# Performance work log

Hardware: AMD Instinct MI355X
Metric: run time of the kernel (lower is better)

Reference implementation:

```python
import jax, jax.numpy as jnp
import numpy as np

B, N1, N2, D = 4, 4096, 4096, 128


def setup_inputs() -> dict:
    key = jax.random.key(0)
    k1, k2 = jax.random.split(key)
    x1 = jax.random.normal(k1, (B, N1, D), dtype=jnp.float32)
    x2 = jax.random.normal(k2, (B, N2, D), dtype=jnp.float32)
    return {"x1": x1, "x2": x2}


def reference(x1, x2):
    # torch.cdist(x2, x1, p=2.0): pairwise euclidean distances [B, N2, N1]
    # Expansion form: ||a||^2 + ||b||^2 - 2 a.b  (single GEMM, no [B,N2,N1,D] intermediate)
    sq2 = jnp.sum(x2 * x2, axis=-1)                      # [B, N2]
    sq1 = jnp.sum(x1 * x1, axis=-1)                      # [B, N1]
    inner = jnp.einsum('bnd,bmd->bnm', x2, x1)           # [B, N2, N1]
    sq = sq2[:, :, None] + sq1[:, None, :] - 2.0 * inner
    corr_mat = jnp.sqrt(jnp.maximum(sq, 0.0))            # clamp numerical negatives
    max_ind21 = jnp.argmin(corr_mat, axis=-1)            # [B, N2] nearest x1 for each x2
    max_ind12 = jnp.argmin(corr_mat, axis=-2)            # [B, N1] nearest x2 for each x1
    return (x1, x2, corr_mat, max_ind12, max_ind21)
```

## Files before the change

kernel.cpp:

```cpp
#include <hip/hip_runtime.h>
#include <stdint.h>
#include <stddef.h>

#define BB 4
#define NN 4096
#define DD 128

typedef _Float16 f16;
typedef _Float16 f16x8 __attribute__((ext_vector_type(8)));
typedef float f32x4 __attribute__((ext_vector_type(4)));

__device__ __forceinline__ void gl16(const f16* g, f16* l) {
  __builtin_amdgcn_global_load_lds(
      (const __attribute__((address_space(1))) unsigned int*)g,
      (__attribute__((address_space(3))) unsigned int*)l,
      16, 0, 0);
}

__device__ __forceinline__ float fast_sqrt(float x) {
  float r;
  asm("v_sqrt_f32 %0, %1" : "=v"(r) : "v"(x));
  return r;
}

__global__ __launch_bounds__(256) void prep_kernel(
    const float* __restrict__ x1, const float* __restrict__ x2,
    f16* __restrict__ x1h, f16* __restrict__ x1l,
    f16* __restrict__ x2h, f16* __restrict__ x2l,
    float* __restrict__ sq1, float* __restrict__ sq2,
    float* __restrict__ out)
{
  int gtid = blockIdx.x * blockDim.x + threadIdx.x;
  int gwave = gtid >> 6;
  int lane = gtid & 63;
  int sub = lane >> 3;
  int j = lane & 7;
  int row = gwave * 8 + sub;
  const float* src; f16* dh; f16* dl; float* sq; float* cpy; int r;
  if (row < BB * NN) {
    r = row; src = x1; dh = x1h; dl = x1l; sq = sq1; cpy = out;
  } else {
    r = row - BB * NN; src = x2; dh = x2h; dl = x2l; sq = sq2;
    cpy = out + (size_t)BB * NN * DD;
  }
  const float* p = src + (size_t)r * DD;
  float acc = 0.0f;
  #pragma unroll
  for (int i = 0; i < DD / 8; ++i) {
    int c = j + i * 8;
    float v = p[c];
    float s = v * v;
    acc = (i == 0) ? s : (acc + s);
    f16 h = (f16)v;
    f16 l = (f16)(v - (float)h);
    dh[(size_t)r * DD + c] = h;
    dl[(size_t)r * DD + c] = l;
    cpy[(size_t)r * DD + c] = v;
  }
  acc = acc + __shfl_xor(acc, 1);
  acc = acc + __shfl_xor(acc, 2);
  acc = acc + __shfl_xor(acc, 4);
  if (j == 0) sq[r] = acc;
}

__global__ __launch_bounds__(512, 4) void cdist_kernel(
    const f16* __restrict__ x1h, const f16* __restrict__ x1l,
    const f16* __restrict__ x2h, const f16* __restrict__ x2l,
    const float* __restrict__ sq1, const float* __restrict__ sq2,
    float* __restrict__ corr,
    float* __restrict__ p21v, int* __restrict__ p21i,
    float* __restrict__ p12v, int* __restrict__ p12i)
{
  __shared__ f16 Ah[128 * 32];
  __shared__ f16 Al[128 * 32];
  __shared__ f16 Bh[128 * 32];
  __shared__ f16 Bl[128 * 32];
  __shared__ float s1s[128];
  __shared__ float s2s[128];

  const int b = blockIdx.z;
  int lin = blockIdx.y * 32 + blockIdx.x;
  lin = (lin & 7) * 128 + (lin >> 3);
  const int sbx = lin & 31;
  const int sby = lin >> 5;
  const int bn1 = sbx * 128;
  const int bn2 = sby * 128;

  const int t = threadIdx.x;
  const int wid = t >> 6;
  const int lane = t & 63;
  const int wm = wid & 1;
  const int wn = wid >> 1;
  const int lr = lane & 15;
  const int lg = lane >> 4;

  const f16* gAh = x1h + (size_t)b * NN * DD;
  const f16* gAl = x1l + (size_t)b * NN * DD;
  const f16* gBh = x2h + (size_t)b * NN * DD;
  const f16* gBl = x2l + (size_t)b * NN * DD;

  if (t < 128) s1s[t] = sq1[(size_t)b * NN + bn1 + t];
  else if (t < 256) s2s[t - 128] = sq2[(size_t)b * NN + bn2 + (t - 128)];

  const int rowc = t >> 2;
  const int kc = (t & 3) ^ (rowc & 3) ^ ((rowc >> 2) & 3);
  const int aoff = bn1 * DD + rowc * DD + kc * 8;
  const int boff = bn2 * DD + rowc * DD + kc * 8;
  const int loff = (wid * 64) * 8;
#define STAGE(k0) do { \
    gl16(gAh + aoff + (k0), &Ah[loff]); \
    gl16(gAl + aoff + (k0), &Al[loff]); \
    gl16(gBh + boff + (k0), &Bh[loff]); \
    gl16(gBl + boff + (k0), &Bl[loff]); } while (0)

  f32x4 acc[4][2];
  #pragma unroll
  for (int m = 0; m < 4; ++m)
    #pragma unroll
    for (int n = 0; n < 2; ++n)
      #pragma unroll
      for (int q = 0; q < 4; ++q) acc[m][n][q] = 0.0f;

  STAGE(0);

  const int lgx8 = (lg ^ (lr & 3) ^ ((lr >> 2) & 3)) * 8;
  const int offA0 = (wm * 64 + lr) * 32 + lgx8;
  const int offB0 = (wn * 32 + lr) * 32 + lgx8;

  for (int it = 0; it < 4; ++it) {
    __syncthreads();
    f16x8 fah[4], fal[4], fbh[2], fbl[2];
    #pragma unroll
    for (int m = 0; m < 4; ++m) {
      fah[m] = *(const f16x8*)&Ah[offA0 + m * 512];
      fal[m] = *(const f16x8*)&Al[offA0 + m * 512];
    }
    #pragma unroll
    for (int n = 0; n < 2; ++n) {
      fbh[n] = *(const f16x8*)&Bh[offB0 + n * 512];
      fbl[n] = *(const f16x8*)&Bl[offB0 + n * 512];
    }
    __syncthreads();
    if (it < 3) STAGE((it + 1) * 32);
    #pragma unroll
    for (int m = 0; m < 4; ++m)
      #pragma unroll
      for (int n = 0; n < 2; ++n) {
        acc[m][n] = __builtin_amdgcn_mfma_f32_16x16x32_f16(fah[m], fbh[n], acc[m][n], 0, 0, 0);
        acc[m][n] = __builtin_amdgcn_mfma_f32_16x16x32_f16(fah[m], fbl[n], acc[m][n], 0, 0, 0);
        acc[m][n] = __builtin_amdgcn_mfma_f32_16x16x32_f16(fal[m], fbh[n], acc[m][n], 0, 0, 0);
      }
  }
#undef STAGE

  float s2r[2];
  #pragma unroll
  for (int n = 0; n < 2; ++n) s2r[n] = s2s[wn * 32 + n * 16 + lr];
  float s1r[4][4];
  #pragma unroll
  for (int m = 0; m < 4; ++m)
    #pragma unroll
    for (int q = 0; q < 4; ++q) s1r[m][q] = s1s[wm * 64 + m * 16 + lg * 4 + q];

  float v21[2]; int i21[2];
  #pragma unroll
  for (int n = 0; n < 2; ++n) { v21[n] = 3.4e38f; i21[n] = 0; }

  float* cbp = corr + (size_t)b * NN * NN;
  #pragma unroll
  for (int m = 0; m < 4; ++m) {
    const int n1b = wm * 64 + m * 16 + lg * 4;
    float v12[4]; int i12[4];
    #pragma unroll
    for (int q = 0; q < 4; ++q) { v12[q] = 3.4e38f; i12[q] = 0; }
    #pragma unroll
    for (int n = 0; n < 2; ++n) {
      const int n2l = wn * 32 + n * 16 + lr;
      f32x4 dv;
      float sqc[4];
      #pragma unroll
      for (int q = 0; q < 4; ++q) {
        const float sv = fmaxf(fmaf(-2.0f, acc[m][n][q], s1r[m][q] + s2r[n]), 0.0f);
        sqc[q] = sv;
        dv[q] = fast_sqrt(sv);
      }
      __builtin_nontemporal_store(dv, (f32x4*)(cbp + (size_t)(bn2 + n2l) * NN + (bn1 + n1b)));
      #pragma unroll
      for (int q = 0; q < 4; ++q) {
        if (sqc[q] < v21[n]) { v21[n] = sqc[q]; i21[n] = bn1 + n1b + q; }
        if (sqc[q] < v12[q]) { v12[q] = sqc[q]; i12[q] = bn2 + n2l; }
      }
    }
    #pragma unroll
    for (int q = 0; q < 4; ++q) {
      float v = v12[q]; int idx = i12[q];
      #pragma unroll
      for (int mask = 1; mask < 16; mask <<= 1) {
        float ov = __shfl_xor(v, mask);
        int oi = __shfl_xor(idx, mask);
        if (ov < v || (ov == v && oi < idx)) { v = ov; idx = oi; }
      }
      if (lr == 0) {
        const int colg = bn1 + n1b + q;
        const size_t o = ((size_t)b * NN + colg) * 128 + (sby * 4 + wn);
        p12v[o] = v; p12i[o] = idx;
      }
    }
  }
  #pragma unroll
  for (int n = 0; n < 2; ++n) {
    float v = v21[n]; int idx = i21[n];
    #pragma unroll
    for (int mask = 16; mask < 64; mask <<= 1) {
      float ov = __shfl_xor(v, mask);
      int oi = __shfl_xor(idx, mask);
      if (ov < v || (ov == v && oi < idx)) { v = ov; idx = oi; }
    }
    if (lg == 0) {
      const int rowg = bn2 + wn * 32 + n * 16 + lr;
      const size_t o = ((size_t)b * NN + rowg) * 64 + (sbx * 2 + wm);
      p21v[o] = v; p21i[o] = idx;
    }
  }
}

__global__ __launch_bounds__(256) void argmin_reduce_kernel(
    const float* __restrict__ p21v, const int* __restrict__ p21i,
    const float* __restrict__ p12v, const int* __restrict__ p12i,
    float* __restrict__ out_i12, float* __restrict__ out_i21)
{
  int gtid = blockIdx.x * blockDim.x + threadIdx.x;
  int gwave = gtid >> 6;
  int lane = gtid & 63;
  float v; int idx; float* dst; int r;
  if (gwave < BB * NN) {
    r = gwave;
    v = p21v[(size_t)r * 64 + lane];
    idx = p21i[(size_t)r * 64 + lane];
    dst = out_i21;
  } else {
    r = gwave - BB * NN;
    v = p12v[(size_t)r * 128 + lane];
    idx = p12i[(size_t)r * 128 + lane];
    float v2 = p12v[(size_t)r * 128 + 64 + lane];
    int i2 = p12i[(size_t)r * 128 + 64 + lane];
    if (v2 < v || (v2 == v && i2 < idx)) { v = v2; idx = i2; }
    dst = out_i12;
  }
  #pragma unroll
  for (int mask = 1; mask < 64; mask <<= 1) {
    float ov = __shfl_xor(v, mask);
    int oi = __shfl_xor(idx, mask);
    if (ov < v || (ov == v && oi < idx)) { v = ov; idx = oi; }
  }
  if (lane == 0) dst[r] = (float)idx;
}

extern "C" void kernel_launch(void* const* d_in, const int* in_sizes, int n_in,
                              void* d_out, int out_size, void* d_ws, size_t ws_size,
                              hipStream_t stream) {
  (void)in_sizes; (void)n_in; (void)out_size; (void)ws_size;
  const float* x1 = (const float*)d_in[0];
  const float* x2 = (const float*)d_in[1];
  float* out = (float*)d_out;
  char* ws = (char*)d_ws;
  const size_t nd = (size_t)BB * NN * DD;
  const size_t bn = (size_t)BB * NN;

  f16* x1h = (f16*)(ws + 0 * nd * 2);
  f16* x1l = (f16*)(ws + 1 * nd * 2);
  f16* x2h = (f16*)(ws + 2 * nd * 2);
  f16* x2l = (f16*)(ws + 3 * nd * 2);
  float* sq1 = (float*)(ws + 4 * nd * 2);
  float* sq2 = (float*)(ws + 4 * nd * 2 + bn * 4);
  char* pbase = ws + 4 * nd * 2 + 2 * bn * 4;
  float* p21v = (float*)(pbase);
  int*   p21i = (int*)  (pbase + 1 * bn * 64 * 4);
  float* p12v = (float*)(pbase + 2 * bn * 64 * 4);
  int*   p12i = (int*)  (pbase + 2 * bn * 64 * 4 + bn * 128 * 4);

  hipLaunchKernelGGL(prep_kernel, dim3(1024), dim3(256), 0, stream,
                     x1, x2, x1h, x1l, x2h, x2l, sq1, sq2, out);

  float* corr = out + 2 * nd;
  hipLaunchKernelGGL(cdist_kernel, dim3(32, 32, 4), dim3(512), 0, stream,
                     x1h, x1l, x2h, x2l, sq1, sq2, corr, p21v, p21i, p12v, p12i);

  float* out_i12 = out + 2 * nd + bn * (size_t)NN;
  float* out_i21 = out_i12 + bn;
  hipLaunchKernelGGL(argmin_reduce_kernel, dim3(8192), dim3(256), 0, stream,
                     p21v, p21i, p12v, p12i, out_i12, out_i21);
}
```

Baseline: 152.2 us.

## Enlarge cdist block tile to 256x128 and pack argmin partials as value-index pairs

The block tile along N1 doubles from 128 to 256, and each wave now computes a 64x64 sub-tile instead of 64x32. This raises MFMA work per LDS fragment load and halves the number of blocks and partial argmin entries. Partial min values and indices are packed into float2 pairs and stored in a transposed layout, so the reduce kernel reads one coalesced 8-byte element per lane. The cost is more accumulator registers and LDS per block, with launch bounds lowered from 4 to 3 blocks per CU, which reduces occupancy.

```diff
diff --git a/kernel.cpp b/kernel.cpp
--- a/kernel.cpp
+++ b/kernel.cpp
@@ -9,6 +9,7 @@
 typedef _Float16 f16;
 typedef _Float16 f16x8 __attribute__((ext_vector_type(8)));
 typedef float f32x4 __attribute__((ext_vector_type(4)));
+typedef float f32x2 __attribute__((ext_vector_type(2)));
 
 __device__ __forceinline__ void gl16(const f16* g, f16* l) {
   __builtin_amdgcn_global_load_lds(
@@ -63,34 +64,33 @@
   if (j == 0) sq[r] = acc;
 }
 
-__global__ __launch_bounds__(512, 4) void cdist_kernel(
+__global__ __launch_bounds__(512, 3) void cdist_kernel(
     const f16* __restrict__ x1h, const f16* __restrict__ x1l,
     const f16* __restrict__ x2h, const f16* __restrict__ x2l,
     const float* __restrict__ sq1, const float* __restrict__ sq2,
     float* __restrict__ corr,
-    float* __restrict__ p21v, int* __restrict__ p21i,
-    float* __restrict__ p12v, int* __restrict__ p12i)
+    f32x2* __restrict__ p21, f32x2* __restrict__ p12)
 {
-  __shared__ f16 Ah[128 * 32];
-  __shared__ f16 Al[128 * 32];
+  __shared__ f16 Ah[256 * 32];
+  __shared__ f16 Al[256 * 32];
   __shared__ f16 Bh[128 * 32];
   __shared__ f16 Bl[128 * 32];
-  __shared__ float s1s[128];
+  __shared__ float s1s[256];
   __shared__ float s2s[128];
 
   const int b = blockIdx.z;
-  int lin = blockIdx.y * 32 + blockIdx.x;
-  lin = (lin & 7) * 128 + (lin >> 3);
-  const int sbx = lin & 31;
-  const int sby = lin >> 5;
-  const int bn1 = sbx * 128;
+  int lin = blockIdx.y * 16 + blockIdx.x;
+  lin = (lin & 7) * 64 + (lin >> 3);
+  const int sbx = lin & 15;
+  const int sby = lin >> 4;
+  const int bn1 = sbx * 256;
   const int bn2 = sby * 128;
 
   const int t = threadIdx.x;
-  const int wid = t >> 6;
+  const int wa = t >> 6;
   const int lane = t & 63;
-  const int wm = wid & 1;
-  const int wn = wid >> 1;
+  const int w1 = wa & 3;
+  const int w2 = wa >> 2;
   const int lr = lane & 15;
   const int lg = lane >> 4;
 
@@ -99,44 +99,54 @@
   const f16* gBh = x2h + (size_t)b * NN * DD;
   const f16* gBl = x2l + (size_t)b * NN * DD;
 
-  if (t < 128) s1s[t] = sq1[(size_t)b * NN + bn1 + t];
-  else if (t < 256) s2s[t - 128] = sq2[(size_t)b * NN + bn2 + (t - 128)];
-
-  const int rowc = t >> 2;
-  const int kc = (t & 3) ^ (rowc & 3) ^ ((rowc >> 2) & 3);
-  const int aoff = bn1 * DD + rowc * DD + kc * 8;
-  const int boff = bn2 * DD + rowc * DD + kc * 8;
-  const int loff = (wid * 64) * 8;
+  if (t < 256) s1s[t] = sq1[(size_t)b * NN + bn1 + t];
+  else if (t < 384) s2s[t - 256] = sq2[(size_t)b * NN + bn2 + (t - 256)];
+
+  int aoff_[2];
+  #pragma unroll
+  for (int r = 0; r < 2; ++r) {
+    const int c = r * 512 + t;
+    const int rowc = c >> 2;
+    const int kc = (c & 3) ^ (rowc & 3) ^ ((rowc >> 2) & 3);
+    aoff_[r] = (bn1 + rowc) * DD + kc * 8;
+  }
+  const int browc = t >> 2;
+  const int bkc = (t & 3) ^ (browc & 3) ^ ((browc >> 2) & 3);
+  const int boff = (bn2 + browc) * DD + bkc * 8;
+  const int lofA0 = (wa * 64) * 8;
+  const int lofA1 = (512 + wa * 64) * 8;
 #define STAGE(k0) do { \
-    gl16(gAh + aoff + (k0), &Ah[loff]); \
-    gl16(gAl + aoff + (k0), &Al[loff]); \
-    gl16(gBh + boff + (k0), &Bh[loff]); \
-    gl16(gBl + boff + (k0), &Bl[loff]); } while (0)
-
-  f32x4 acc[4][2];
+    gl16(gAh + aoff_[0] + (k0), &Ah[lofA0]); \
+    gl16(gAh + aoff_[1] + (k0), &Ah[lofA1]); \
+    gl16(gAl + aoff_[0] + (k0), &Al[lofA0]); \
+    gl16(gAl + aoff_[1] + (k0), &Al[lofA1]); \
+    gl16(gBh + boff + (k0), &Bh[lofA0]); \
+    gl16(gBl + boff + (k0), &Bl[lofA0]); } while (0)
+
+  f32x4 acc[4][4];
   #pragma unroll
   for (int m = 0; m < 4; ++m)
     #pragma unroll
-    for (int n = 0; n < 2; ++n)
+    for (int n = 0; n < 4; ++n)
       #pragma unroll
       for (int q = 0; q < 4; ++q) acc[m][n][q] = 0.0f;
 
   STAGE(0);
 
   const int lgx8 = (lg ^ (lr & 3) ^ ((lr >> 2) & 3)) * 8;
-  const int offA0 = (wm * 64 + lr) * 32 + lgx8;
-  const int offB0 = (wn * 32 + lr) * 32 + lgx8;
+  const int offA0 = (w1 * 64 + lr) * 32 + lgx8;
+  const int offB0 = (w2 * 64 + lr) * 32 + lgx8;
 
   for (int it = 0; it < 4; ++it) {
     __syncthreads();
-    f16x8 fah[4], fal[4], fbh[2], fbl[2];
+    f16x8 fah[4], fal[4], fbh[4], fbl[4];
     #pragma unroll
     for (int m = 0; m < 4; ++m) {
       fah[m] = *(const f16x8*)&Ah[offA0 + m * 512];
       fal[m] = *(const f16x8*)&Al[offA0 + m * 512];
     }
     #pragma unroll
-    for (int n = 0; n < 2; ++n) {
+    for (int n = 0; n < 4; ++n) {
       fbh[n] = *(const f16x8*)&Bh[offB0 + n * 512];
       fbl[n] = *(const f16x8*)&Bl[offB0 + n * 512];
     }
@@ -145,7 +155,7 @@
     #pragma unroll
     for (int m = 0; m < 4; ++m)
       #pragma unroll
-      for (int n = 0; n < 2; ++n) {
+      for (int n = 0; n < 4; ++n) {
         acc[m][n] = __builtin_amdgcn_mfma_f32_16x16x32_f16(fah[m], fbh[n], acc[m][n], 0, 0, 0);
         acc[m][n] = __builtin_amdgcn_mfma_f32_16x16x32_f16(fah[m], fbl[n], acc[m][n], 0, 0, 0);
         acc[m][n] = __builtin_amdgcn_mfma_f32_16x16x32_f16(fal[m], fbh[n], acc[m][n], 0, 0, 0);
@@ -153,29 +163,29 @@
   }
 #undef STAGE
 
-  float s2r[2];
-  #pragma unroll
-  for (int n = 0; n < 2; ++n) s2r[n] = s2s[wn * 32 + n * 16 + lr];
+  float s2r[4];
+  #pragma unroll
+  for (int n = 0; n < 4; ++n) s2r[n] = s2s[w2 * 64 + n * 16 + lr];
   float s1r[4][4];
   #pragma unroll
   for (int m = 0; m < 4; ++m)
     #pragma unroll
-    for (int q = 0; q < 4; ++q) s1r[m][q] = s1s[wm * 64 + m * 16 + lg * 4 + q];
-
-  float v21[2]; int i21[2];
-  #pragma unroll
-  for (int n = 0; n < 2; ++n) { v21[n] = 3.4e38f; i21[n] = 0; }
+    for (int q = 0; q < 4; ++q) s1r[m][q] = s1s[w1 * 64 + m * 16 + lg * 4 + q];
+
+  float v21[4]; int i21[4];
+  #pragma unroll
+  for (int n = 0; n < 4; ++n) { v21[n] = 3.4e38f; i21[n] = 0; }
 
   float* cbp = corr + (size_t)b * NN * NN;
   #pragma unroll
   for (int m = 0; m < 4; ++m) {
-    const int n1b = wm * 64 + m * 16 + lg * 4;
+    const int n1b = bn1 + w1 * 64 + m * 16 + lg * 4;
     float v12[4]; int i12[4];
     #pragma unroll
     for (int q = 0; q < 4; ++q) { v12[q] = 3.4e38f; i12[q] = 0; }
     #pragma unroll
-    for (int n = 0; n < 2; ++n) {
-      const int n2l = wn * 32 + n * 16 + lr;
+    for (int n = 0; n < 4; ++n) {
+      const int n2g = bn2 + w2 * 64 + n * 16 + lr;
       f32x4 dv;
       float sqc[4];
       #pragma unroll
@@ -184,11 +194,11 @@
         sqc[q] = sv;
         dv[q] = fast_sqrt(sv);
       }
-      __builtin_nontemporal_store(dv, (f32x4*)(cbp + (size_t)(bn2 + n2l) * NN + (bn1 + n1b)));
+      __builtin_nontemporal_store(dv, (f32x4*)(cbp + (size_t)n2g * NN + n1b));
       #pragma unroll
       for (int q = 0; q < 4; ++q) {
-        if (sqc[q] < v21[n]) { v21[n] = sqc[q]; i21[n] = bn1 + n1b + q; }
-        if (sqc[q] < v12[q]) { v12[q] = sqc[q]; i12[q] = bn2 + n2l; }
+        if (sqc[q] < v21[n]) { v21[n] = sqc[q]; i21[n] = n1b + q; }
+        if (sqc[q] < v12[q]) { v12[q] = sqc[q]; i12[q] = n2g; }
       }
     }
     #pragma unroll
@@ -201,14 +211,13 @@
         if (ov < v || (ov == v && oi < idx)) { v = ov; idx = oi; }
       }
       if (lr == 0) {
-        const int colg = bn1 + n1b + q;
-        const size_t o = ((size_t)b * NN + colg) * 128 + (sby * 4 + wn);
-        p12v[o] = v; p12i[o] = idx;
-      }
-    }
-  }
-  #pragma unroll
-  for (int n = 0; n < 2; ++n) {
+        const size_t o = (size_t)((b * 32 + sby) * 2 + w2) * NN + (n1b + q);
+        p12[o] = f32x2{v, __int_as_float(idx)};
+      }
+    }
+  }
+  #pragma unroll
+  for (int n = 0; n < 4; ++n) {
     float v = v21[n]; int idx = i21[n];
     #pragma unroll
     for (int mask = 16; mask < 64; mask <<= 1) {
@@ -217,36 +226,33 @@
       if (ov < v || (ov == v && oi < idx)) { v = ov; idx = oi; }
     }
     if (lg == 0) {
-      const int rowg = bn2 + wn * 32 + n * 16 + lr;
-      const size_t o = ((size_t)b * NN + rowg) * 64 + (sbx * 2 + wm);
-      p21v[o] = v; p21i[o] = idx;
+      const int rowg = bn2 + w2 * 64 + n * 16 + lr;
+      const size_t o = (size_t)((b * 16 + sbx) * 4 + w1) * NN + rowg;
+      p21[o] = f32x2{v, __int_as_float(idx)};
     }
   }
 }
 
 __global__ __launch_bounds__(256) void argmin_reduce_kernel(
-    const float* __restrict__ p21v, const int* __restrict__ p21i,
-    const float* __restrict__ p12v, const int* __restrict__ p12i,
+    const f32x2* __restrict__ p21, const f32x2* __restrict__ p12,
     float* __restrict__ out_i12, float* __restrict__ out_i21)
 {
   int gtid = blockIdx.x * blockDim.x + threadIdx.x;
   int gwave = gtid >> 6;
   int lane = gtid & 63;
-  float v; int idx; float* dst; int r;
+  f32x2 e; float* dst; int r;
   if (gwave < BB * NN) {
     r = gwave;
-    v = p21v[(size_t)r * 64 + lane];
-    idx = p21i[(size_t)r * 64 + lane];
+    const int b = r >> 12, row = r & (NN - 1);
+    e = p21[(size_t)((b * 16 + (lane >> 2)) * 4 + (lane & 3)) * NN + row];
     dst = out_i21;
   } else {
     r = gwave - BB * NN;
-    v = p12v[(size_t)r * 128 + lane];
-    idx = p12i[(size_t)r * 128 + lane];
-    float v2 = p12v[(size_t)r * 128 + 64 + lane];
-    int i2 = p12i[(size_t)r * 128 + 64 + lane];
-    if (v2 < v || (v2 == v && i2 < idx)) { v = v2; idx = i2; }
+    const int b = r >> 12, col = r & (NN - 1);
+    e = p12[(size_t)((b * 32 + (lane >> 1)) * 2 + (lane & 1)) * NN + col];
     dst = out_i12;
   }
+  float v = e[0]; int idx = __float_as_int(e[1]);
   #pragma unroll
   for (int mask = 1; mask < 64; mask <<= 1) {
     float ov = __shfl_xor(v, mask);
@@ -273,21 +279,18 @@
   f16* x2l = (f16*)(ws + 3 * nd * 2);
   float* sq1 = (float*)(ws + 4 * nd * 2);
   float* sq2 = (float*)(ws + 4 * nd * 2 + bn * 4);
-  char* pbase = ws + 4 * nd * 2 + 2 * bn * 4;
-  float* p21v = (float*)(pbase);
-  int*   p21i = (int*)  (pbase + 1 * bn * 64 * 4);
-  float* p12v = (float*)(pbase + 2 * bn * 64 * 4);
-  int*   p12i = (int*)  (pbase + 2 * bn * 64 * 4 + bn * 128 * 4);
+  f32x2* p21 = (f32x2*)(ws + 4 * nd * 2 + 2 * bn * 4);
+  f32x2* p12 = (f32x2*)(ws + 4 * nd * 2 + 2 * bn * 4 + bn * 64 * 8);
 
   hipLaunchKernelGGL(prep_kernel, dim3(1024), dim3(256), 0, stream,
                      x1, x2, x1h, x1l, x2h, x2l, sq1, sq2, out);
 
   float* corr = out + 2 * nd;
-  hipLaunchKernelGGL(cdist_kernel, dim3(32, 32, 4), dim3(512), 0, stream,
-                     x1h, x1l, x2h, x2l, sq1, sq2, corr, p21v, p21i, p12v, p12i);
+  hipLaunchKernelGGL(cdist_kernel, dim3(16, 32, 4), dim3(512), 0, stream,
+                     x1h, x1l, x2h, x2l, sq1, sq2, corr, p21, p12);
 
   float* out_i12 = out + 2 * nd + bn * (size_t)NN;
   float* out_i21 = out_i12 + bn;
   hipLaunchKernelGGL(argmin_reduce_kernel, dim3(8192), dim3(256), 0, stream,
-                     p21v, p21i, p12v, p12i, out_i12, out_i21);
-}
+                     p21, p12, out_i12, out_i21);
+}
```

Result: slower. 158.7 us (+4.3%).
